# Optimization experiments

Measured on AMD Instinct MI355X. Metric: run time of the kernel, lower is better.

The kernel has to match this reference:

```python
import jax, jax.numpy as jnp
import numpy as np

# dims: N patches, D_IN input feats, D model, DI=inner, DS=state, DC=conv, DTR=dt_rank
N, D_IN, D, DI, DS, DC, DTR, NC, NL = 4096, 1024, 512, 1024, 16, 4, 32, 4, 2


def setup_inputs() -> dict:
    key = jax.random.key(0)
    ks = jax.random.split(key, 16)
    g = lambda i, shape, s=0.02: jax.random.normal(ks[i], shape, dtype=jnp.float32) * s
    return {
        "data_s": jax.random.normal(ks[0], (N, 512), dtype=jnp.float32),
        "data_l": jax.random.normal(ks[1], (N, 512), dtype=jnp.float32),
        "coord_s": jax.random.uniform(ks[2], (N, 2), dtype=jnp.float32) * 1000.0,
        "label": jax.random.randint(ks[3], (1,), 0, NC),
        "fc1_w": g(4, (D, D_IN)), "fc1_b": jnp.zeros((D,), jnp.float32),
        "ln_w": jnp.ones((NL, D), jnp.float32), "ln_b": jnp.zeros((NL, D), jnp.float32),
        "in_proj_w": g(5, (NL, 2 * DI, D)),
        "conv_w": g(6, (NL, DI, DC), 0.1), "conv_b": jnp.zeros((NL, DI), jnp.float32),
        "x_proj_w": g(7, (NL, DTR + 2 * DS, DI)),
        "dt_proj_w": g(8, (NL, DI, DTR), 0.1), "dt_proj_b": g(9, (NL, DI), 0.5),
        "A_log": jnp.broadcast_to(jnp.log(jnp.arange(1, DS + 1, dtype=jnp.float32)), (NL, DI, DS)) + jnp.zeros((NL, DI, DS), jnp.float32),
        "D_param": jnp.ones((NL, DI), jnp.float32),
        "out_proj_w": g(10, (NL, D, DI)),
        "norm_w": jnp.ones((D,), jnp.float32), "norm_b": jnp.zeros((D,), jnp.float32),
        "attn_w1": g(11, (128, D)), "attn_b1": jnp.zeros((128,), jnp.float32),
        "attn_w2": g(12, (1, 128)), "attn_b2": jnp.zeros((1,), jnp.float32),
        "cls_w": g(13, (NC, D)), "cls_b": jnp.zeros((NC,), jnp.float32),
    }


def _layer_norm(x, w, b, eps=1e-5):
    m = x.mean(-1, keepdims=True)
    v = ((x - m) ** 2).mean(-1, keepdims=True)
    return (x - m) * jax.lax.rsqrt(v + eps) * w + b


def _mamba(h, inw, cw, cb, xpw, dtw, dtb, Alog, Dp, ow):
    # h: (B, L, D) -> (B, L, D); canonical Mamba block (mamba_ssm defaults)
    B, L, _ = h.shape
    xz = h @ inw.T                      # (B, L, 2*DI)
    x, z = jnp.split(xz, 2, axis=-1)
    # causal depthwise conv1d, kernel DC, left pad DC-1 (== torch pad+truncate)
    xp = jnp.pad(x, ((0, 0), (DC - 1, 0), (0, 0)))
    x = sum(xp[:, k:k + L, :] * cw[:, k] for k in range(DC)) + cb
    x = jax.nn.silu(x)
    xdbl = x @ xpw.T                    # (B, L, DTR + 2*DS)
    dt, Bm, Cm = jnp.split(xdbl, [DTR, DTR + DS], axis=-1)
    dt = jax.nn.softplus(dt @ dtw.T + dtb)   # (B, L, DI)
    A = -jnp.exp(Alog)                  # (DI, DS)
    dA = jnp.exp(dt[..., None] * A)                          # (B, L, DI, DS)
    dBx = dt[..., None] * Bm[:, :, None, :] * x[..., None]   # (B, L, DI, DS)

    def step(hst, inp):
        dA_t, dBx_t, C_t = inp
        hst = dA_t * hst + dBx_t        # (B, DI, DS)
        return hst, jnp.einsum('bds,bs->bd', hst, C_t)

    h0 = jnp.zeros((B, DI, DS), x.dtype)
    _, ys = jax.lax.scan(step, h0, (jnp.swapaxes(dA, 0, 1), jnp.swapaxes(dBx, 0, 1), jnp.swapaxes(Cm, 0, 1)))
    y = jnp.swapaxes(ys, 0, 1) + Dp * x
    return (y * jax.nn.silu(z)) @ ow.T


def _forward(data_s, data_l, coord_s, fc1_w, fc1_b, ln_w, ln_b, in_proj_w, conv_w, conv_b,
             x_proj_w, dt_proj_w, dt_proj_b, A_log, D_param, out_proj_w, norm_w, norm_b,
             attn_w1, attn_b1, attn_w2, attn_b2, cls_w, cls_b, label):
    h = jnp.concatenate([data_s, data_l], axis=1)            # (N, 1024)
    packed = jnp.concatenate([h, coord_s], axis=1)[None]     # (1, N, 1026)
    h = packed[:, :, :-2]                                    # strip coords
    h = jax.nn.relu(h @ fc1_w.T + fc1_b)                     # dropout: eval mode (identity)
    for i in range(NL):
        res = h
        hn = _layer_norm(h, ln_w[i], ln_b[i])
        h = _mamba(hn, in_proj_w[i], conv_w[i], conv_b[i], x_proj_w[i], dt_proj_w[i],
                   dt_proj_b[i], A_log[i], D_param[i], out_proj_w[i]) + res
    h = _layer_norm(h, norm_w, norm_b)
    A = jnp.tanh(h @ attn_w1.T + attn_b1) @ attn_w2.T + attn_b2   # (1, N, 1)
    A = jax.nn.softmax(jnp.swapaxes(A, 1, 2), axis=-1)            # (1, 1, N)
    hp = (A @ h)[0]                                               # (1, D)
    logits = hp @ cls_w.T + cls_b                                 # (1, NC)
    hz = jax.nn.sigmoid(logits)
    p = jnp.clip(hz, 1e-6, 1.0 - 1e-6)
    lce = jnp.log(p) - jnp.log1p(-p)                              # torch.logit
    Y_prob = jax.nn.softmax(lce, axis=1)
    loss = -jnp.take(jax.nn.log_softmax(lce, axis=1)[0], label[0])
    return lce, Y_prob, loss


def reference(data_s, data_l, coord_s, label, fc1_w, fc1_b, ln_w, ln_b, in_proj_w, conv_w,
              conv_b, x_proj_w, dt_proj_w, dt_proj_b, A_log, D_param, out_proj_w, norm_w,
              norm_b, attn_w1, attn_b1, attn_w2, attn_b2, cls_w, cls_b):
    return _forward(data_s, data_l, coord_s, fc1_w, fc1_b, ln_w, ln_b, in_proj_w, conv_w,
                    conv_b, x_proj_w, dt_proj_w, dt_proj_b, A_log, D_param, out_proj_w,
                    norm_w, norm_b, attn_w1, attn_b1, attn_w2, attn_b2, cls_w, cls_b, label)
```

## Files before the change

kernel.cpp:

```cpp
#include <hip/hip_runtime.h>
#include <math.h>

#define L_SEQ 4096
#define DMODEL 512
#define DIN    1024
#define DI     1024
#define DS     16
#define DC     4
#define DTR    32
#define NCHK   512
#define CL     8
#define NPAIR  (DI * DS)
#define NG     32
#define GS     16
#define SLAB   (L_SEQ * 64)

typedef __bf16 bf16x8 __attribute__((ext_vector_type(8)));
typedef __bf16 bf16x4 __attribute__((ext_vector_type(4)));
typedef float floatx4 __attribute__((ext_vector_type(4)));

#define RLN2 1.44269504f
#define LN2  0.69314718f

__device__ __forceinline__ float softplus_fast(float x) {
    if (x > 20.f) return x;
    float e = __builtin_amdgcn_exp2f(x * RLN2);
    return LN2 * __builtin_amdgcn_logf(1.f + e);
}

__device__ __forceinline__ void gl2lds16(const __bf16* g, __bf16* l) {
    __builtin_amdgcn_global_load_lds(
        (const __attribute__((address_space(1))) void*)g,
        (__attribute__((address_space(3))) void*)l, 16, 0, 0);
}

template <int BN, int ACT, bool BIAS, bool ADDDEST, bool OUTBF, int KS>
__global__ __launch_bounds__(256) void gemm_mfma(
    const __bf16* __restrict__ A, int lda,
    const __bf16* __restrict__ W, int ldw,
    const float* __restrict__ bias,
    float* __restrict__ C, __bf16* __restrict__ Cb, int ldc, int K)
{
    __shared__ __align__(16) __bf16 sA[128 * 32];
    __shared__ __align__(16) __bf16 sB[BN * 32];
    const int tid = threadIdx.x;
    const int wid = tid >> 6, lane = tid & 63;
    const int m0 = blockIdx.y * 128;
    int n0;
    if (KS > 1) {
        const int ksl = blockIdx.x;
        A += (size_t)ksl * K;
        W += (size_t)ksl * K;
        C += (size_t)ksl * (size_t)gridDim.y * 128 * ldc;
        n0 = 0;
    } else {
        n0 = blockIdx.x * BN;
    }

    constexpr int MR = (BN == 128) ? 4 : 2;
    constexpr int NR = 4;
    const int wrow = (BN == 128) ? (wid >> 1) * 64 : wid * 32;
    const int wcol = (BN == 128) ? (wid & 1) * 64 : 0;

    const int srowA0 = wid * 32 + (lane >> 2);
    const int scol   = (lane & 3) * 8;
    const __bf16* aSrc0 = A + (size_t)(m0 + srowA0) * lda + scol;
    const __bf16* aSrc1 = aSrc0 + 16 * (size_t)lda;
    __bf16* aDst0 = &sA[wid * 1024];
    __bf16* aDst1 = &sA[wid * 1024 + 512];

    const __bf16* bSrc0;
    const __bf16* bSrc1 = nullptr;
    __bf16* bDst0;
    __bf16* bDst1 = nullptr;
    if (BN == 128) {
        bSrc0 = W + (size_t)(n0 + wid * 32 + (lane >> 2)) * ldw + scol;
        bSrc1 = bSrc0 + 16 * (size_t)ldw;
        bDst0 = &sB[wid * 1024];
        bDst1 = &sB[wid * 1024 + 512];
    } else {
        bSrc0 = W + (size_t)(n0 + wid * 16 + (lane >> 2)) * ldw + scol;
        bDst0 = &sB[wid * 512];
    }

    floatx4 acc[MR][NR] = {};
    const int fr = lane & 15;
    const int fk = (lane >> 4) * 8;

    for (int k0 = 0; k0 < K; k0 += 32) {
        __syncthreads();
        gl2lds16(aSrc0 + k0, aDst0);
        gl2lds16(aSrc1 + k0, aDst1);
        gl2lds16(bSrc0 + k0, bDst0);
        if (BN == 128) gl2lds16(bSrc1 + k0, bDst1);
        __syncthreads();
        bf16x8 af[MR], bfv[NR];
#pragma unroll
        for (int i = 0; i < MR; ++i)
            af[i] = *(const bf16x8*)&sA[(wrow + i * 16 + fr) * 32 + fk];
#pragma unroll
        for (int j = 0; j < NR; ++j)
            bfv[j] = *(const bf16x8*)&sB[(wcol + j * 16 + fr) * 32 + fk];
#pragma unroll
        for (int i = 0; i < MR; ++i)
#pragma unroll
            for (int j = 0; j < NR; ++j)
                acc[i][j] = __builtin_amdgcn_mfma_f32_16x16x32_bf16(
                    af[i], bfv[j], acc[i][j], 0, 0, 0);
    }

#pragma unroll
    for (int i = 0; i < MR; ++i)
#pragma unroll
        for (int j = 0; j < NR; ++j) {
            const int n = n0 + wcol + j * 16 + fr;
            float bv = 0.f;
            if (BIAS) bv = bias[n];
#pragma unroll
            for (int r = 0; r < 4; ++r) {
                const int m = m0 + wrow + i * 16 + (lane >> 4) * 4 + r;
                float v = acc[i][j][r] + bv;
                if (ACT == 1) v = fmaxf(v, 0.f);
                else if (ACT == 2) v = tanhf(v);
                const size_t idx = (size_t)m * ldc + n;
                if (OUTBF) {
                    Cb[idx] = (__bf16)v;
                } else {
                    if (ADDDEST) v += C[idx];
                    C[idx] = v;
                }
            }
        }
}

__global__ void prep_k(const float* __restrict__ s0, __bf16* __restrict__ d0, int n0,
                       const float* __restrict__ s1, __bf16* __restrict__ d1, int n1,
                       const float* __restrict__ s2, __bf16* __restrict__ d2, int n2,
                       const float* __restrict__ s3, __bf16* __restrict__ d3, int n3,
                       const float* __restrict__ s4, __bf16* __restrict__ d4, int n4,
                       const float* __restrict__ dtw, float* __restrict__ dtwT, int n5,
                       const float* __restrict__ Alog, float* __restrict__ As2T, int n6)
{
    int i = blockIdx.x * 256 + threadIdx.x;
    int tot = n0 + n1 + n2 + n3 + n4;
    if (i >= tot) {
        int j = i - tot;
        if (j < n5) {
            int l = j >> 15, rem = j & 32767, r = rem >> 5, k = rem & 31;
            dtwT[l * 32768 + k * 1024 + r] = dtw[j];
        } else if (j - n5 < n6) {
            int k = j - n5;
            As2T[k] = -__expf(Alog[k]) * RLN2;
        }
        return;
    }
    const float* s; __bf16* d; int base;
    if (i < n0) { s = s0; d = d0; base = i; }
    else if (i < n0 + n1) { s = s1; d = d1; base = i - n0; }
    else if (i < n0 + n1 + n2) { s = s2; d = d2; base = i - n0 - n1; }
    else if (i < n0 + n1 + n2 + n3) { s = s3; d = d3; base = i - n0 - n1 - n2; }
    else { s = s4; d = d4; base = i - n0 - n1 - n2 - n3; }
    float4 a = ((const float4*)s)[2 * base], b = ((const float4*)s)[2 * base + 1];
    bf16x8 v;
    v[0] = (__bf16)a.x; v[1] = (__bf16)a.y; v[2] = (__bf16)a.z; v[3] = (__bf16)a.w;
    v[4] = (__bf16)b.x; v[5] = (__bf16)b.y; v[6] = (__bf16)b.z; v[7] = (__bf16)b.w;
    *(bf16x8*)&d[8 * base] = v;
}

__global__ void concat_bf_k(const float* __restrict__ a,
                            const float* __restrict__ b,
                            __bf16* __restrict__ o)
{
    int idx = blockIdx.x * 256 + threadIdx.x;
    int m = idx >> 7, c8 = (idx & 127) << 3;
    const float* src = (c8 < 512) ? &a[(m << 9) + c8] : &b[(m << 9) + c8 - 512];
    float4 x = ((const float4*)src)[0], y = ((const float4*)src)[1];
    bf16x8 v;
    v[0] = (__bf16)x.x; v[1] = (__bf16)x.y; v[2] = (__bf16)x.z; v[3] = (__bf16)x.w;
    v[4] = (__bf16)y.x; v[5] = (__bf16)y.y; v[6] = (__bf16)y.z; v[7] = (__bf16)y.w;
    *(bf16x8*)&o[idx << 3] = v;
}

template <int OMODE>
__global__ __launch_bounds__(128) void layernorm_k(
    const float* __restrict__ X, const float* __restrict__ w,
    const float* __restrict__ b, float* __restrict__ Yf, __bf16* __restrict__ Yb)
{
    const int r = blockIdx.x, tid = threadIdx.x;
    const size_t base = ((size_t)r << 9) + (tid << 2);
    const float4 v = *(const float4*)&X[base];
    float s = v.x + v.y + v.z + v.w;
#pragma unroll
    for (int o = 32; o; o >>= 1) s += __shfl_down(s, o, 64);
    __shared__ float red[2];
    if ((tid & 63) == 0) red[tid >> 6] = s;
    __syncthreads();
    const float mean = (red[0] + red[1]) * (1.f / 512.f);
    float dx = v.x - mean, dy = v.y - mean, dz = v.z - mean, dw = v.w - mean;
    float q = dx * dx + dy * dy + dz * dz + dw * dw;
#pragma unroll
    for (int o = 32; o; o >>= 1) q += __shfl_down(q, o, 64);
    __shared__ float red2[2];
    if ((tid & 63) == 0) red2[tid >> 6] = q;
    __syncthreads();
    const float rs = rsqrtf((red2[0] + red2[1]) * (1.f / 512.f) + 1e-5f);
    const float4 wv = *(const float4*)&w[tid << 2];
    const float4 bv = *(const float4*)&b[tid << 2];
    float o0 = dx * rs * wv.x + bv.x;
    float o1 = dy * rs * wv.y + bv.y;
    float o2 = dz * rs * wv.z + bv.z;
    float o3 = dw * rs * wv.w + bv.w;
    if (OMODE != 1) {
        float4 ov; ov.x = o0; ov.y = o1; ov.z = o2; ov.w = o3;
        *(float4*)&Yf[base] = ov;
    }
    if (OMODE != 0) {
        bf16x4 ov; ov[0] = (__bf16)o0; ov[1] = (__bf16)o1;
        ov[2] = (__bf16)o2; ov[3] = (__bf16)o3;
        *(bf16x4*)&Yb[base] = ov;
    }
}

__global__ void conv_silu_k(const __bf16* __restrict__ XZb,
                            const float* __restrict__ cw,
                            const float* __restrict__ cb,
                            __bf16* __restrict__ XCb)
{
    int i = blockIdx.x * 256 + threadIdx.x;
    int t = i >> 8, d4 = (i & 255) << 2;
    float wt[4][4];
#pragma unroll
    for (int d = 0; d < 4; ++d) {
        float4 w = *(const float4*)&cw[(d4 + d) << 2];
        wt[d][0] = w.x; wt[d][1] = w.y; wt[d][2] = w.z; wt[d][3] = w.w;
    }
    float4 c = *(const float4*)&cb[d4];
    float a0 = c.x, a1 = c.y, a2 = c.z, a3 = c.w;
#pragma unroll
    for (int k = 0; k < 4; ++k) {
        int ts = t + k - 3;
        if (ts >= 0) {
            bf16x4 x = *(const bf16x4*)&XZb[((size_t)ts << 11) + d4];
            a0 = fmaf((float)x[0], wt[0][k], a0);
            a1 = fmaf((float)x[1], wt[1][k], a1);
            a2 = fmaf((float)x[2], wt[2][k], a2);
            a3 = fmaf((float)x[3], wt[3][k], a3);
        }
    }
    a0 *= 1.f / (1.f + __expf(-a0));
    a1 *= 1.f / (1.f + __expf(-a1));
    a2 *= 1.f / (1.f + __expf(-a2));
    a3 *= 1.f / (1.f + __expf(-a3));
    bf16x4 ob; ob[0] = (__bf16)a0; ob[1] = (__bf16)a1;
    ob[2] = (__bf16)a2; ob[3] = (__bf16)a3;
    *(bf16x4*)&XCb[((size_t)t << 10) + d4] = ob;
}

__global__ __launch_bounds__(256) void scanA_k(
    const __bf16* __restrict__ xc, const float* __restrict__ xdblP,
    const float* __restrict__ dtwT, const float* __restrict__ dtb,
    const float* __restrict__ As2T,
    __bf16* __restrict__ dtsum, __bf16* __restrict__ sH,
    __bf16* __restrict__ dtg)
{
    const int d = blockIdx.x * 256 + threadIdx.x;
    const int c = blockIdx.y;
    const int tid = threadIdx.x;
    __shared__ float xlow[CL][DTR];
    __shared__ float Bs[CL][DS];
    __shared__ float dts[CL][256];
    {
        int t = tid >> 5, k = tid & 31;
        size_t g = (size_t)(c * CL + t) * 64 + k;
        xlow[t][k] = xdblP[g] + xdblP[SLAB + g] + xdblP[2 * SLAB + g] + xdblP[3 * SLAB + g];
    }
    if (tid < CL * DS) {
        int t = tid >> 4, s = tid & 15;
        size_t g = (size_t)(c * CL + t) * 64 + 32 + s;
        Bs[t][s] = xdblP[g] + xdblP[SLAB + g] + xdblP[2 * SLAB + g] + xdblP[3 * SLAB + g];
    }
    __syncthreads();
    float dtw_d[32];
#pragma unroll
    for (int k = 0; k < 32; ++k) dtw_d[k] = dtwT[k * 1024 + d];
    const float dtb_d = dtb[d];
    float sumdt = 0.f;
#pragma unroll
    for (int t = 0; t < CL; ++t) {
        float p0 = 0.f, p1 = 0.f, p2 = 0.f, p3 = 0.f;
#pragma unroll
        for (int k4 = 0; k4 < 8; ++k4) {
            float4 xq = *(const float4*)&xlow[t][k4 * 4];
            p0 = fmaf(xq.x, dtw_d[k4 * 4 + 0], p0);
            p1 = fmaf(xq.y, dtw_d[k4 * 4 + 1], p1);
            p2 = fmaf(xq.z, dtw_d[k4 * 4 + 2], p2);
            p3 = fmaf(xq.w, dtw_d[k4 * 4 + 3], p3);
        }
        float acc = ((p0 + p1) + (p2 + p3)) + dtb_d;
        float dtv = softplus_fast(acc);
        dts[t][tid] = dtv;
        dtg[((size_t)(c * CL + t) << 10) + d] = (__bf16)dtv;
        sumdt += dtv;
    }
    dtsum[(size_t)c * DI + d] = (__bf16)sumdt;
    float As2[DS], h[DS];
    {
        const float4* Ap4 = (const float4*)&As2T[(size_t)d * DS];
#pragma unroll
        for (int q = 0; q < 4; ++q) {
            float4 a = Ap4[q];
            As2[q * 4 + 0] = a.x; As2[q * 4 + 1] = a.y;
            As2[q * 4 + 2] = a.z; As2[q * 4 + 3] = a.w;
        }
    }
#pragma unroll
    for (int s = 0; s < DS; ++s) h[s] = 0.f;
    for (int t = 0; t < CL; ++t) {
        float dtv = dts[t][tid];
        float xv = (float)xc[((size_t)(c * CL + t) << 10) + d];
        float dx = dtv * xv;
        float barr[16];
#pragma unroll
        for (int q = 0; q < 4; ++q) {
            float4 b = *(const float4*)&Bs[t][q * 4];
            barr[q * 4 + 0] = b.x; barr[q * 4 + 1] = b.y;
            barr[q * 4 + 2] = b.z; barr[q * 4 + 3] = b.w;
        }
#pragma unroll
        for (int s = 0; s < DS; ++s) {
            float a = exp2f(dtv * As2[s]);
            h[s] = fmaf(a, h[s], dx * barr[s]);
        }
    }
    size_t base = ((size_t)c * DI + d) * DS;
    bf16x8 h0v, h1v;
#pragma unroll
    for (int s = 0; s < 8; ++s) {
        h0v[s] = (__bf16)h[s];
        h1v[s] = (__bf16)h[s + 8];
    }
    *(bf16x8*)&sH[base] = h0v; *(bf16x8*)&sH[base + 8] = h1v;
}

__global__ __launch_bounds__(256) void scanB1_k(
    const __bf16* __restrict__ dtsum, const __bf16* __restrict__ sH,
    const float* __restrict__ As2T,
    __bf16* __restrict__ PG, __bf16* __restrict__ HG)
{
    int p = blockIdx.x * 256 + threadIdx.x;
    int g = blockIdx.y;
    const int d = p >> 4;
    const float as2 = As2T[p];
    float rp = 1.f, rh = 0.f;
#pragma unroll
    for (int k = 0; k < GS; ++k) {
        int c = g * GS + k;
        float P = exp2f(as2 * (float)dtsum[(size_t)c * DI + d]);
        float H = (float)sH[(size_t)c * NPAIR + p];
        rh = fmaf(P, rh, H);
        rp *= P;
    }
    PG[(size_t)g * NPAIR + p] = (__bf16)rp;
    HG[(size_t)g * NPAIR + p] = (__bf16)rh;
}

__global__ __launch_bounds__(256) void scanB2_k(
    const __bf16* __restrict__ PG, const __bf16* __restrict__ HG,
    __bf16* __restrict__ Gin)
{
    int p = blockIdx.x * 256 + threadIdx.x;
    float run = 0.f;
#pragma unroll
    for (int g = 0; g < NG; ++g) {
        size_t idx = (size_t)g * NPAIR + p;
        Gin[idx] = (__bf16)run;
        run = fmaf((float)PG[idx], run, (float)HG[idx]);
    }
}

__global__ __launch_bounds__(256) void scanB3_k(
    const __bf16* __restrict__ dtsum, const __bf16* __restrict__ sH,
    const float* __restrict__ As2T,
    const __bf16* __restrict__ Gin, __bf16* __restrict__ Hin)
{
    int p = blockIdx.x * 256 + threadIdx.x;
    int g = blockIdx.y;
    const int d = p >> 4;
    const float as2 = As2T[p];
    float run = (float)Gin[(size_t)g * NPAIR + p];
#pragma unroll
    for (int k = 0; k < GS; ++k) {
        int c = g * GS + k;
        size_t idx = (size_t)c * NPAIR + p;
        Hin[idx] = (__bf16)run;
        float P = exp2f(as2 * (float)dtsum[(size_t)c * DI + d]);
        run = fmaf(P, run, (float)sH[idx]);
    }
}

__global__ __launch_bounds__(256) void scanC_k(
    const __bf16* __restrict__ xc, const float* __restrict__ xdblP,
    const __bf16* __restrict__ dtg, const float* __restrict__ As2T,
    const float* __restrict__ Dp, const __bf16* __restrict__ XZb,
    const __bf16* __restrict__ Hin, __bf16* __restrict__ yz)
{
    const int d = blockIdx.x * 256 + threadIdx.x;
    const int c = blockIdx.y;
    const int tid = threadIdx.x;
    __shared__ float Bs[CL][DS], Cs[CL][DS];
    if (tid < CL * DS) {
        int t = tid >> 4, s = tid & 15;
        size_t g = (size_t)(c * CL + t) * 64 + 32 + s;
        Bs[t][s] = xdblP[g] + xdblP[SLAB + g] + xdblP[2 * SLAB + g] + xdblP[3 * SLAB + g];
        g += 16;
        Cs[t][s] = xdblP[g] + xdblP[SLAB + g] + xdblP[2 * SLAB + g] + xdblP[3 * SLAB + g];
    }
    __syncthreads();
    float As2[DS], h[DS];
    {
        const float4* Ap4 = (const float4*)&As2T[(size_t)d * DS];
#pragma unroll
        for (int q = 0; q < 4; ++q) {
            float4 a = Ap4[q];
            As2[q * 4 + 0] = a.x; As2[q * 4 + 1] = a.y;
            As2[q * 4 + 2] = a.z; As2[q * 4 + 3] = a.w;
        }
    }
    {
        size_t base = ((size_t)c * DI + d) * DS;
        bf16x8 h0 = *(const bf16x8*)&Hin[base];
        bf16x8 h1 = *(const bf16x8*)&Hin[base + 8];
#pragma unroll
        for (int s = 0; s < 8; ++s) { h[s] = (float)h0[s]; h[s + 8] = (float)h1[s]; }
    }
    const float Dd = Dp[d];
    for (int t = 0; t < CL; ++t) {
        size_t tg = (size_t)(c * CL + t);
        const float dtv = (float)dtg[(tg << 10) + d];
        const float xv = (float)xc[(tg << 10) + d];
        const float dx = dtv * xv;
        float barr[16], carr[16];
#pragma unroll
        for (int q = 0; q < 4; ++q) {
            float4 b = *(const float4*)&Bs[t][q * 4];
            float4 cc = *(const float4*)&Cs[t][q * 4];
            barr[q * 4 + 0] = b.x; barr[q * 4 + 1] = b.y;
            barr[q * 4 + 2] = b.z; barr[q * 4 + 3] = b.w;
            carr[q * 4 + 0] = cc.x; carr[q * 4 + 1] = cc.y;
            carr[q * 4 + 2] = cc.z; carr[q * 4 + 3] = cc.w;
        }
        float y = 0.f;
#pragma unroll
        for (int s = 0; s < DS; ++s) {
            float a = exp2f(dtv * As2[s]);
            h[s] = fmaf(a, h[s], dx * barr[s]);
            y = fmaf(h[s], carr[s], y);
        }
        y = fmaf(Dd, xv, y);
        float zv = (float)XZb[(tg << 11) + 1024 + d];
        float sg = 1.f / (1.f + __expf(-zv));
        yz[(tg << 10) + d] = (__bf16)(y * (zv * sg));
    }
}

__global__ void score_k(const float* __restrict__ At,
                        const float* __restrict__ w2,
                        const float* __restrict__ b2,
                        float* __restrict__ sc)
{
    int t = blockIdx.x * 256 + threadIdx.x;
    const float4* a = (const float4*)(At + ((size_t)t << 7));
    const float4* w = (const float4*)w2;
    float acc = 0.f;
#pragma unroll
    for (int j = 0; j < 32; ++j) {
        float4 av = a[j], wv = w[j];
        acc += av.x * wv.x + av.y * wv.y + av.z * wv.z + av.w * wv.w;
    }
    sc[t] = acc + b2[0];
}

__global__ __launch_bounds__(256) void softmax_k(const float* __restrict__ s,
                                                 float* __restrict__ p)
{
    const int tid = threadIdx.x;
    float vals[16];
#pragma unroll
    for (int i = 0; i < 4; ++i) {
        float4 v = *(const float4*)&s[(tid << 4) + (i << 2)];
        vals[i * 4 + 0] = v.x; vals[i * 4 + 1] = v.y;
        vals[i * 4 + 2] = v.z; vals[i * 4 + 3] = v.w;
    }
    float mx = -1e30f;
#pragma unroll
    for (int i = 0; i < 16; ++i) mx = fmaxf(mx, vals[i]);
#pragma unroll
    for (int o = 32; o; o >>= 1) mx = fmaxf(mx, __shfl_xor(mx, o, 64));
    __shared__ float red[4];
    if ((tid & 63) == 0) red[tid >> 6] = mx;
    __syncthreads();
    mx = fmaxf(fmaxf(red[0], red[1]), fmaxf(red[2], red[3]));
    float sum = 0.f, e[16];
#pragma unroll
    for (int i = 0; i < 16; ++i) { e[i] = __expf(vals[i] - mx); sum += e[i]; }
#pragma unroll
    for (int o = 32; o; o >>= 1) sum += __shfl_xor(sum, o, 64);
    __syncthreads();
    if ((tid & 63) == 0) red[tid >> 6] = sum;
    __syncthreads();
    sum = red[0] + red[1] + red[2] + red[3];
    float inv = 1.f / sum;
#pragma unroll
    for (int i = 0; i < 4; ++i) {
        float4 ov;
        ov.x = e[i * 4 + 0] * inv; ov.y = e[i * 4 + 1] * inv;
        ov.z = e[i * 4 + 2] * inv; ov.w = e[i * 4 + 3] * inv;
        *(float4*)&p[(tid << 4) + (i << 2)] = ov;
    }
}

__global__ void pool_partial_k(const float* __restrict__ prob,
                               const float* __restrict__ hln,
                               float* __restrict__ part)
{
    int j = blockIdx.x * 256 + threadIdx.x;
    int c = blockIdx.y;
    float acc = 0.f;
    for (int t = c * 128; t < (c + 1) * 128; ++t)
        acc = fmaf(prob[t], hln[((size_t)t << 9) + j], acc);
    part[c * 512 + j] = acc;
}

__global__ void pool_reduce_k(const float* __restrict__ part,
                              float* __restrict__ hp)
{
    int j = blockIdx.x * 256 + threadIdx.x;
    float acc = 0.f;
    for (int c = 0; c < 32; ++c) acc += part[c * 512 + j];
    hp[j] = acc;
}

__global__ __launch_bounds__(256) void final_head_k(
    const float* __restrict__ hp, const float* __restrict__ cls_w,
    const float* __restrict__ cls_b, const int* __restrict__ label,
    float* __restrict__ out)
{
    const int w = threadIdx.x >> 6, lane = threadIdx.x & 63;
    float acc = 0.f;
    for (int k = lane; k < 512; k += 64) acc += hp[k] * cls_w[w * 512 + k];
#pragma unroll
    for (int o = 32; o; o >>= 1) acc += __shfl_down(acc, o, 64);
    __shared__ float lg[4];
    if (lane == 0) lg[w] = acc + cls_b[w];
    __syncthreads();
    if (threadIdx.x == 0) {
        float lce[4];
        for (int c = 0; c < 4; ++c) {
            float z = lg[c];
            float hz = 1.f / (1.f + expf(-z));
            float pc = fminf(fmaxf(hz, 1e-6f), 1.f - 1e-6f);
            lce[c] = logf(pc) - log1pf(-pc);
        }
        float mx = fmaxf(fmaxf(lce[0], lce[1]), fmaxf(lce[2], lce[3]));
        float se = 0.f;
        for (int c = 0; c < 4; ++c) se += expf(lce[c] - mx);
        for (int c = 0; c < 4; ++c) out[c] = lce[c];
        for (int c = 0; c < 4; ++c) out[4 + c] = expf(lce[c] - mx) / se;
        int lb = label[0];
        out[8] = -(lce[lb] - mx - logf(se));
    }
}

extern "C" void kernel_launch(void* const* d_in, const int* in_sizes, int n_in,
                              void* d_out, int out_size, void* d_ws, size_t ws_size,
                              hipStream_t stream)
{
    const float* data_s   = (const float*)d_in[0];
    const float* data_l   = (const float*)d_in[1];
    const int*   label    = (const int*)d_in[3];
    const float* fc1_w    = (const float*)d_in[4];
    const float* fc1_b    = (const float*)d_in[5];
    const float* ln_w     = (const float*)d_in[6];
    const float* ln_b     = (const float*)d_in[7];
    const float* in_proj_w= (const float*)d_in[8];
    const float* conv_w   = (const float*)d_in[9];
    const float* conv_b   = (const float*)d_in[10];
    const float* x_proj_w = (const float*)d_in[11];
    const float* dt_proj_w= (const float*)d_in[12];
    const float* dt_proj_b= (const float*)d_in[13];
    const float* A_log    = (const float*)d_in[14];
    const float* D_param  = (const float*)d_in[15];
    const float* out_proj_w=(const float*)d_in[16];
    const float* norm_w   = (const float*)d_in[17];
    const float* norm_b   = (const float*)d_in[18];
    const float* attn_w1  = (const float*)d_in[19];
    const float* attn_b1  = (const float*)d_in[20];
    const float* attn_w2  = (const float*)d_in[21];
    const float* attn_b2  = (const float*)d_in[22];
    const float* cls_w    = (const float*)d_in[23];
    const float* cls_b    = (const float*)d_in[24];
    float* out = (float*)d_out;

    float* ws = (float*)d_ws;
    size_t off = 0;
    float* h     = ws + off; off += (size_t)L_SEQ * DMODEL;
    float* hn    = ws + off; off += (size_t)L_SEQ * DMODEL;
    float* xdblP = ws + off; off += (size_t)4 * SLAB;
    float* dtwT  = ws + off; off += (size_t)2 * DTR * DI;
    float* As2T  = ws + off; off += (size_t)2 * DI * DS;
    float* At    = ws + off; off += (size_t)L_SEQ * 128;
    float* sc    = ws + off; off += L_SEQ;
    float* pb    = ws + off; off += L_SEQ;
    float* part  = ws + off; off += 32 * 512;
    float* hp    = ws + off; off += 512;

    __bf16* bws = (__bf16*)(ws + off);
    size_t boff = 0;
    __bf16* Acatb = bws + boff; boff += (size_t)L_SEQ * DIN;
    __bf16* hnb   = bws + boff; boff += (size_t)L_SEQ * DMODEL;
    __bf16* XZb   = bws + boff; boff += (size_t)L_SEQ * 2 * DI;
    __bf16* XCb   = bws + boff; boff += (size_t)L_SEQ * DI;
    __bf16* yzb   = bws + boff; boff += (size_t)L_SEQ * DI;
    __bf16* sHb   = bws + boff; boff += (size_t)NCHK * NPAIR;
    __bf16* HinB  = bws + boff; boff += (size_t)NCHK * NPAIR;
    __bf16* dtgB  = bws + boff; boff += (size_t)L_SEQ * DI;
    __bf16* dtsumB= bws + boff; boff += (size_t)NCHK * DI;
    __bf16* PGb   = bws + boff; boff += (size_t)NG * NPAIR;
    __bf16* HGb   = bws + boff; boff += (size_t)NG * NPAIR;
    __bf16* GinB  = bws + boff; boff += (size_t)NG * NPAIR;
    __bf16* wfc1b = bws + boff; boff += (size_t)DMODEL * DIN;
    __bf16* winb  = bws + boff; boff += (size_t)2 * 2 * DI * DMODEL;
    __bf16* wxpb  = bws + boff; boff += (size_t)2 * 64 * DI;
    __bf16* woutb = bws + boff; boff += (size_t)2 * DMODEL * DI;
    __bf16* w1b   = bws + boff; boff += (size_t)128 * DMODEL;
    if (ws_size < off * sizeof(float) + boff * sizeof(__bf16)) return;

    const int n0 = DMODEL * DIN / 8;
    const int n1 = 2 * 2 * DI * DMODEL / 8;
    const int n2 = 2 * 64 * DI / 8;
    const int n3 = 2 * DMODEL * DI / 8;
    const int n4 = 128 * DMODEL / 8;
    const int n5 = 2 * DI * DTR;
    const int n6 = 2 * DI * DS;
    prep_k<<<(n0 + n1 + n2 + n3 + n4 + n5 + n6 + 255) / 256, 256, 0, stream>>>(
        fc1_w, wfc1b, n0, in_proj_w, winb, n1, x_proj_w, wxpb, n2,
        out_proj_w, woutb, n3, attn_w1, w1b, n4, dt_proj_w, dtwT, n5,
        A_log, As2T, n6);

    concat_bf_k<<<L_SEQ * DIN / 8 / 256, 256, 0, stream>>>(data_s, data_l, Acatb);
    gemm_mfma<64, 1, true, false, false, 1><<<dim3(DMODEL / 64, L_SEQ / 128), 256, 0, stream>>>(
        Acatb, DIN, wfc1b, DIN, fc1_b, h, nullptr, DMODEL, DIN);

    for (int i = 0; i < 2; ++i) {
        const __bf16* inw = winb + (size_t)i * 2 * DI * DMODEL;
        const float* cwi = conv_w + (size_t)i * DI * DC;
        const float* cbi = conv_b + (size_t)i * DI;
        const __bf16* xpw = wxpb + (size_t)i * 64 * DI;
        const float* dtwTi = dtwT + (size_t)i * DTR * DI;
        const float* dtbv= dt_proj_b + (size_t)i * DI;
        const float* As2i = As2T + (size_t)i * DI * DS;
        const float* Dpi = D_param + (size_t)i * DI;
        const __bf16* owi = woutb + (size_t)i * DMODEL * DI;

        layernorm_k<1><<<L_SEQ, 128, 0, stream>>>(h, ln_w + i * DMODEL, ln_b + i * DMODEL, nullptr, hnb);
        gemm_mfma<128, 0, false, false, true, 1><<<dim3(2 * DI / 128, L_SEQ / 128), 256, 0, stream>>>(
            hnb, DMODEL, inw, DMODEL, nullptr, nullptr, XZb, 2 * DI, DMODEL);
        conv_silu_k<<<L_SEQ * DI / 4 / 256, 256, 0, stream>>>(XZb, cwi, cbi, XCb);
        gemm_mfma<64, 0, false, false, false, 4><<<dim3(4, L_SEQ / 128), 256, 0, stream>>>(
            XCb, DI, xpw, DI, nullptr, xdblP, nullptr, 64, DI / 4);
        scanA_k<<<dim3(DI / 256, NCHK), 256, 0, stream>>>(
            XCb, xdblP, dtwTi, dtbv, As2i, dtsumB, sHb, dtgB);
        scanB1_k<<<dim3(NPAIR / 256, NG), 256, 0, stream>>>(dtsumB, sHb, As2i, PGb, HGb);
        scanB2_k<<<NPAIR / 256, 256, 0, stream>>>(PGb, HGb, GinB);
        scanB3_k<<<dim3(NPAIR / 256, NG), 256, 0, stream>>>(dtsumB, sHb, As2i, GinB, HinB);
        scanC_k<<<dim3(DI / 256, NCHK), 256, 0, stream>>>(
            XCb, xdblP, dtgB, As2i, Dpi, XZb, HinB, yzb);
        gemm_mfma<64, 0, false, true, false, 1><<<dim3(DMODEL / 64, L_SEQ / 128), 256, 0, stream>>>(
            yzb, DI, owi, DI, nullptr, h, nullptr, DMODEL, DI);
    }

    layernorm_k<2><<<L_SEQ, 128, 0, stream>>>(h, norm_w, norm_b, hn, hnb);
    gemm_mfma<64, 2, true, false, false, 1><<<dim3(2, L_SEQ / 128), 256, 0, stream>>>(
        hnb, DMODEL, w1b, DMODEL, attn_b1, At, nullptr, 128, DMODEL);
    score_k<<<L_SEQ / 256, 256, 0, stream>>>(At, attn_w2, attn_b2, sc);
    softmax_k<<<1, 256, 0, stream>>>(sc, pb);
    pool_partial_k<<<dim3(2, 32), 256, 0, stream>>>(pb, hn, part);
    pool_reduce_k<<<2, 256, 0, stream>>>(part, hp);
    final_head_k<<<1, 256, 0, stream>>>(hp, cls_w, cls_b, label, out);
}
```

Baseline: 405.5 us.

## Fold dt_proj into x_proj weights and compute dt via a dense MFMA GEMM

```diff
diff --git a/kernel.cpp b/kernel.cpp
--- a/kernel.cpp
+++ b/kernel.cpp
@@ -122,6 +122,7 @@
                 float v = acc[i][j][r] + bv;
                 if (ACT == 1) v = fmaxf(v, 0.f);
                 else if (ACT == 2) v = tanhf(v);
+                else if (ACT == 3) v = softplus_fast(v);
                 const size_t idx = (size_t)m * ldc + n;
                 if (OUTBF) {
                     Cb[idx] = (__bf16)v;
@@ -138,20 +139,13 @@
                        const float* __restrict__ s2, __bf16* __restrict__ d2, int n2,
                        const float* __restrict__ s3, __bf16* __restrict__ d3, int n3,
                        const float* __restrict__ s4, __bf16* __restrict__ d4, int n4,
-                       const float* __restrict__ dtw, float* __restrict__ dtwT, int n5,
                        const float* __restrict__ Alog, float* __restrict__ As2T, int n6)
 {
     int i = blockIdx.x * 256 + threadIdx.x;
     int tot = n0 + n1 + n2 + n3 + n4;
     if (i >= tot) {
-        int j = i - tot;
-        if (j < n5) {
-            int l = j >> 15, rem = j & 32767, r = rem >> 5, k = rem & 31;
-            dtwT[l * 32768 + k * 1024 + r] = dtw[j];
-        } else if (j - n5 < n6) {
-            int k = j - n5;
-            As2T[k] = -__expf(Alog[k]) * RLN2;
-        }
+        int k = i - tot;
+        if (k < n6) As2T[k] = -__expf(Alog[k]) * RLN2;
         return;
     }
     const float* s; __bf16* d; int base;
@@ -167,6 +161,38 @@
     *(bf16x8*)&d[8 * base] = v;
 }
 
+__global__ __launch_bounds__(256) void w2_k(
+    const float* __restrict__ dtw, const float* __restrict__ xpw,
+    __bf16* __restrict__ W2)
+{
+    const int tid = threadIdx.x;
+    const int kbase = blockIdx.x * 256;
+    const int dbase = blockIdx.y * 64;
+    const int l = blockIdx.z;
+    __shared__ float xpw_s[32][256];
+    __shared__ float dtw_s[64][32];
+#pragma unroll
+    for (int u = 0; u < 32; ++u) {
+        int e = u * 256 + tid;
+        int r = e >> 8, k = e & 255;
+        xpw_s[r][k] = xpw[(size_t)l * 65536 + r * 1024 + kbase + k];
+    }
+#pragma unroll
+    for (int u = 0; u < 8; ++u) {
+        int e = u * 256 + tid;
+        int dd = e >> 5, r = e & 31;
+        dtw_s[dd][r] = dtw[(size_t)l * 32768 + (dbase + dd) * 32 + r];
+    }
+    __syncthreads();
+    for (int dd = 0; dd < 64; ++dd) {
+        float acc = 0.f;
+#pragma unroll
+        for (int r = 0; r < 32; ++r)
+            acc = fmaf(dtw_s[dd][r], xpw_s[r][tid], acc);
+        W2[(size_t)l * 1048576 + (size_t)(dbase + dd) * 1024 + kbase + tid] = (__bf16)acc;
+    }
+}
+
 __global__ void concat_bf_k(const float* __restrict__ a,
                             const float* __restrict__ b,
                             __bf16* __restrict__ o)
@@ -258,51 +284,19 @@
 
 __global__ __launch_bounds__(256) void scanA_k(
     const __bf16* __restrict__ xc, const float* __restrict__ xdblP,
-    const float* __restrict__ dtwT, const float* __restrict__ dtb,
-    const float* __restrict__ As2T,
-    __bf16* __restrict__ dtsum, __bf16* __restrict__ sH,
-    __bf16* __restrict__ dtg)
+    const __bf16* __restrict__ dtg, const float* __restrict__ As2T,
+    __bf16* __restrict__ dtsum, __bf16* __restrict__ sH)
 {
     const int d = blockIdx.x * 256 + threadIdx.x;
     const int c = blockIdx.y;
     const int tid = threadIdx.x;
-    __shared__ float xlow[CL][DTR];
     __shared__ float Bs[CL][DS];
-    __shared__ float dts[CL][256];
-    {
-        int t = tid >> 5, k = tid & 31;
-        size_t g = (size_t)(c * CL + t) * 64 + k;
-        xlow[t][k] = xdblP[g] + xdblP[SLAB + g] + xdblP[2 * SLAB + g] + xdblP[3 * SLAB + g];
-    }
     if (tid < CL * DS) {
         int t = tid >> 4, s = tid & 15;
         size_t g = (size_t)(c * CL + t) * 64 + 32 + s;
         Bs[t][s] = xdblP[g] + xdblP[SLAB + g] + xdblP[2 * SLAB + g] + xdblP[3 * SLAB + g];
     }
     __syncthreads();
-    float dtw_d[32];
-#pragma unroll
-    for (int k = 0; k < 32; ++k) dtw_d[k] = dtwT[k * 1024 + d];
-    const float dtb_d = dtb[d];
-    float sumdt = 0.f;
-#pragma unroll
-    for (int t = 0; t < CL; ++t) {
-        float p0 = 0.f, p1 = 0.f, p2 = 0.f, p3 = 0.f;
-#pragma unroll
-        for (int k4 = 0; k4 < 8; ++k4) {
-            float4 xq = *(const float4*)&xlow[t][k4 * 4];
-            p0 = fmaf(xq.x, dtw_d[k4 * 4 + 0], p0);
-            p1 = fmaf(xq.y, dtw_d[k4 * 4 + 1], p1);
-            p2 = fmaf(xq.z, dtw_d[k4 * 4 + 2], p2);
-            p3 = fmaf(xq.w, dtw_d[k4 * 4 + 3], p3);
-        }
-        float acc = ((p0 + p1) + (p2 + p3)) + dtb_d;
-        float dtv = softplus_fast(acc);
-        dts[t][tid] = dtv;
-        dtg[((size_t)(c * CL + t) << 10) + d] = (__bf16)dtv;
-        sumdt += dtv;
-    }
-    dtsum[(size_t)c * DI + d] = (__bf16)sumdt;
     float As2[DS], h[DS];
     {
         const float4* Ap4 = (const float4*)&As2T[(size_t)d * DS];
@@ -315,10 +309,13 @@
     }
 #pragma unroll
     for (int s = 0; s < DS; ++s) h[s] = 0.f;
+    float sumdt = 0.f;
     for (int t = 0; t < CL; ++t) {
-        float dtv = dts[t][tid];
-        float xv = (float)xc[((size_t)(c * CL + t) << 10) + d];
+        size_t tg = (size_t)(c * CL + t);
+        float dtv = (float)dtg[(tg << 10) + d];
+        float xv  = (float)xc[(tg << 10) + d];
         float dx = dtv * xv;
+        sumdt += dtv;
         float barr[16];
 #pragma unroll
         for (int q = 0; q < 4; ++q) {
@@ -332,6 +329,7 @@
             h[s] = fmaf(a, h[s], dx * barr[s]);
         }
     }
+    dtsum[(size_t)c * DI + d] = (__bf16)sumdt;
     size_t base = ((size_t)c * DI + d) * DS;
     bf16x8 h0v, h1v;
 #pragma unroll
@@ -606,7 +604,6 @@
     float* h     = ws + off; off += (size_t)L_SEQ * DMODEL;
     float* hn    = ws + off; off += (size_t)L_SEQ * DMODEL;
     float* xdblP = ws + off; off += (size_t)4 * SLAB;
-    float* dtwT  = ws + off; off += (size_t)2 * DTR * DI;
     float* As2T  = ws + off; off += (size_t)2 * DI * DS;
     float* At    = ws + off; off += (size_t)L_SEQ * 128;
     float* sc    = ws + off; off += L_SEQ;
@@ -633,6 +630,7 @@
     __bf16* wxpb  = bws + boff; boff += (size_t)2 * 64 * DI;
     __bf16* woutb = bws + boff; boff += (size_t)2 * DMODEL * DI;
     __bf16* w1b   = bws + boff; boff += (size_t)128 * DMODEL;
+    __bf16* W2b   = bws + boff; boff += (size_t)2 * DI * DI;
     if (ws_size < off * sizeof(float) + boff * sizeof(__bf16)) return;
 
     const int n0 = DMODEL * DIN / 8;
@@ -640,12 +638,11 @@
     const int n2 = 2 * 64 * DI / 8;
     const int n3 = 2 * DMODEL * DI / 8;
     const int n4 = 128 * DMODEL / 8;
-    const int n5 = 2 * DI * DTR;
     const int n6 = 2 * DI * DS;
-    prep_k<<<(n0 + n1 + n2 + n3 + n4 + n5 + n6 + 255) / 256, 256, 0, stream>>>(
+    prep_k<<<(n0 + n1 + n2 + n3 + n4 + n6 + 255) / 256, 256, 0, stream>>>(
         fc1_w, wfc1b, n0, in_proj_w, winb, n1, x_proj_w, wxpb, n2,
-        out_proj_w, woutb, n3, attn_w1, w1b, n4, dt_proj_w, dtwT, n5,
-        A_log, As2T, n6);
+        out_proj_w, woutb, n3, attn_w1, w1b, n4, A_log, As2T, n6);
+    w2_k<<<dim3(4, 16, 2), 256, 0, stream>>>(dt_proj_w, x_proj_w, W2b);
 
     concat_bf_k<<<L_SEQ * DIN / 8 / 256, 256, 0, stream>>>(data_s, data_l, Acatb);
     gemm_mfma<64, 1, true, false, false, 1><<<dim3(DMODEL / 64, L_SEQ / 128), 256, 0, stream>>>(
@@ -656,7 +653,7 @@
         const float* cwi = conv_w + (size_t)i * DI * DC;
         const float* cbi = conv_b + (size_t)i * DI;
         const __bf16* xpw = wxpb + (size_t)i * 64 * DI;
-        const float* dtwTi = dtwT + (size_t)i * DTR * DI;
+        const __bf16* W2i = W2b + (size_t)i * DI * DI;
         const float* dtbv= dt_proj_b + (size_t)i * DI;
         const float* As2i = As2T + (size_t)i * DI * DS;
         const float* Dpi = D_param + (size_t)i * DI;
@@ -668,8 +665,10 @@
         conv_silu_k<<<L_SEQ * DI / 4 / 256, 256, 0, stream>>>(XZb, cwi, cbi, XCb);
         gemm_mfma<64, 0, false, false, false, 4><<<dim3(4, L_SEQ / 128), 256, 0, stream>>>(
             XCb, DI, xpw, DI, nullptr, xdblP, nullptr, 64, DI / 4);
+        gemm_mfma<64, 3, true, false, true, 1><<<dim3(DI / 64, L_SEQ / 128), 256, 0, stream>>>(
+            XCb, DI, W2i, DI, dtbv, nullptr, dtgB, DI, DI);
         scanA_k<<<dim3(DI / 256, NCHK), 256, 0, stream>>>(
-            XCb, xdblP, dtwTi, dtbv, As2i, dtsumB, sHb, dtgB);
+            XCb, xdblP, dtgB, As2i, dtsumB, sHb);
         scanB1_k<<<dim3(NPAIR / 256, NG), 256, 0, stream>>>(dtsumB, sHb, As2i, PGb, HGb);
         scanB2_k<<<NPAIR / 256, 256, 0, stream>>>(PGb, HGb, GinB);
         scanB3_k<<<dim3(NPAIR / 256, NG), 256, 0, stream>>>(dtsumB, sHb, As2i, GinB, HinB);
```

Measured after the change: 448.4 us. +10.6%, slower.
